# Optimization experiments

Measured on AMD Instinct MI355X. Metric: run time of the kernel, lower is better.

The kernel has to match this reference:

```python
import jax, jax.numpy as jnp
from jax import lax
import numpy as np

NBITS = 3  # PartialSumLSQ bit width


def binarize(x):
    # straight-through sign (Binarize in BNN code modifies .data -> identity STE)
    return x + lax.stop_gradient(jnp.sign(x) - x)


def lsq(y, alpha):
    # LSQ quantizer for partial sums: q = round(clamp(y/a, Qn, Qp)) * a, STE round,
    # gradient-scaled step size (forward value unaffected by g).
    Qn, Qp = -(2 ** (NBITS - 1)), 2 ** (NBITS - 1) - 1
    g = 1.0 / np.sqrt(y.size * Qp)
    a = alpha * g + lax.stop_gradient(alpha - alpha * g)
    yc = jnp.clip(y / a, Qn, Qp)
    yq = yc + lax.stop_gradient(jnp.round(yc) - yc)
    return yq * a


def split_slices(xp, cgroups):
    # xp: [B, 128*cgroups, H+2, W+2]; reproduces split_tensor_128/256/512 ordering:
    # channel group outermost, then col offset j, then row offset i.
    H, W = xp.shape[2] - 2, xp.shape[3] - 2
    sl = [xp[:, g * 128:(g + 1) * 128, i:i + H, j:j + W]
          for g in range(cgroups) for j in range(3) for i in range(3)]
    return jnp.stack(sl)  # [S, B, 128, H, W]


def psum_stage(x, w, b, alpha, cgroups):
    # emulated 3x3 binary conv: pad, split into S shifted 128-ch slices, per-slice
    # binarized 1x1 conv + bias, LSQ-quantize each partial sum, accumulate.
    xp = jnp.pad(binarize(x), ((0, 0), (0, 0), (1, 1), (1, 1)))
    xs = split_slices(xp, cgroups)                      # [S,B,128,H,W]
    y = jnp.einsum('sbchw,soc->sbohw', xs, binarize(w)) + b[:, None, :, None, None]
    return jax.vmap(lsq)(y, alpha).sum(0)               # [B,Cout,H,W]


def maxpool2(x):
    return lax.reduce_window(x, -jnp.inf, lax.max, (1, 1, 2, 2), (1, 1, 2, 2), 'VALID')


def bn(x, g, b):
    # eval-mode BatchNorm with running_mean=0, running_var=1 -> affine
    s = (1, -1) + (1,) * (x.ndim - 2)
    return x * g.reshape(s) + b.reshape(s)


def htanh(x):
    return jnp.clip(x, -1.0, 1.0)


def _forward(x, conv1_w, conv1_b, s2_w, s2_b, s2_a, s3_w, s3_b, s3_a,
             s4_w, s4_b, s4_a, s5_w, s5_b, s5_a, s6_w, s6_b, s6_a,
             bn1_g, bn1_b, bn2_g, bn2_b, bn3_g, bn3_b, bn4_g, bn4_b,
             bn5_g, bn5_b, bn6_g, bn6_b, fc1_w, fc1_b, fc2_w, fc2_b,
             fc3_w, fc3_b, fbn1_g, fbn1_b, fbn2_g, fbn2_b, fbn3_g, fbn3_b):
    # conv1: 3->128 3x3 pad1; input has 3 channels -> not binarized, weight binarized
    h = lax.conv_general_dilated(x, binarize(conv1_w), (1, 1), ((1, 1), (1, 1)),
                                 dimension_numbers=('NCHW', 'OIHW', 'NCHW'))
    h = h + conv1_b[None, :, None, None]
    h = htanh(bn(h, bn1_g, bn1_b))
    h = psum_stage(h, s2_w, s2_b, s2_a, 1)   # 128->128, 9 slices, 32x32
    h = maxpool2(h)                          # 16x16
    h = htanh(bn(h, bn2_g, bn2_b))
    h = psum_stage(h, s3_w, s3_b, s3_a, 1)   # 128->256, 9 slices
    h = htanh(bn(h, bn3_g, bn3_b))
    h = psum_stage(h, s4_w, s4_b, s4_a, 2)   # 256->256, 18 slices
    h = maxpool2(h)                          # 8x8
    h = htanh(bn(h, bn4_g, bn4_b))
    h = psum_stage(h, s5_w, s5_b, s5_a, 2)   # 256->512, 18 slices
    h = htanh(bn(h, bn5_g, bn5_b))
    h = psum_stage(h, s6_w, s6_b, s6_a, 4)   # 512->512, 36 slices
    h = maxpool2(h)                          # 4x4
    h = htanh(bn(h, bn6_g, bn6_b))
    # binarized classifier: 512*4*4 -> 1024 -> 1024 -> num_classes
    f = binarize(h.reshape(h.shape[0], -1))
    f = f @ binarize(fc1_w).T + fc1_b
    f = htanh(f * fbn1_g + fbn1_b)
    f = binarize(f) @ binarize(fc2_w).T + fc2_b
    f = htanh(f * fbn2_g + fbn2_b)
    f = binarize(f) @ binarize(fc3_w).T + fc3_b
    return f * fbn3_g + fbn3_b


def setup_inputs() -> dict:
    key = jax.random.key(0)
    ks = iter(jax.random.split(key, 80))
    def rn(shape, scale=1.0):
        return jax.random.normal(next(ks), shape, jnp.float32) * scale
    d = {}
    d['x'] = rn((64, 3, 32, 32))
    d['conv1_w'] = rn((128, 3, 3, 3), 0.1)
    d['conv1_b'] = rn((128,), 0.01)
    stages = {'s2': (9, 128), 's3': (9, 256), 's4': (18, 256),
              's5': (18, 512), 's6': (36, 512)}
    for name, (S, co) in stages.items():
        d[name + '_w'] = rn((S, co, 128), 0.1)
        d[name + '_b'] = rn((S, co), 0.01)
        d[name + '_a'] = jax.random.uniform(next(ks), (S,), jnp.float32, 0.05, 0.15)
    for i, c in zip(range(1, 7), [128, 128, 256, 256, 512, 512]):
        d[f'bn{i}_g'] = jnp.ones((c,), jnp.float32) + rn((c,), 0.01)
        d[f'bn{i}_b'] = rn((c,), 0.01)
    d['fc1_w'] = rn((1024, 512 * 16), 0.02); d['fc1_b'] = rn((1024,), 0.01)
    d['fc2_w'] = rn((1024, 1024), 0.02);     d['fc2_b'] = rn((1024,), 0.01)
    d['fc3_w'] = rn((10, 1024), 0.02);       d['fc3_b'] = rn((10,), 0.01)
    for i, c in zip(range(1, 4), [1024, 1024, 10]):
        d[f'fbn{i}_g'] = jnp.ones((c,), jnp.float32) + rn((c,), 0.01)
        d[f'fbn{i}_b'] = rn((c,), 0.01)
    return d


def reference(x, conv1_w, conv1_b, s2_w, s2_b, s2_a, s3_w, s3_b, s3_a,
              s4_w, s4_b, s4_a, s5_w, s5_b, s5_a, s6_w, s6_b, s6_a,
              bn1_g, bn1_b, bn2_g, bn2_b, bn3_g, bn3_b, bn4_g, bn4_b,
              bn5_g, bn5_b, bn6_g, bn6_b, fc1_w, fc1_b, fc2_w, fc2_b,
              fc3_w, fc3_b, fbn1_g, fbn1_b, fbn2_g, fbn2_b, fbn3_g, fbn3_b):
    return _forward(x, conv1_w, conv1_b, s2_w, s2_b, s2_a, s3_w, s3_b, s3_a,
                    s4_w, s4_b, s4_a, s5_w, s5_b, s5_a, s6_w, s6_b, s6_a,
                    bn1_g, bn1_b, bn2_g, bn2_b, bn3_g, bn3_b, bn4_g, bn4_b,
                    bn5_g, bn5_b, bn6_g, bn6_b, fc1_w, fc1_b, fc2_w, fc2_b,
                    fc3_w, fc3_b, fbn1_g, fbn1_b, fbn2_g, fbn2_b, fbn3_g, fbn3_b)
```

## Files before the change

### kernel.cpp

```cpp
#include <hip/hip_runtime.h>
#include <hip/hip_bf16.h>

typedef unsigned long long u64;

struct PackArgs {
    const float* w[7];
    u64* out[7];
    int cnt[7];
    int wpr[7];
    int nseg;
    int total;
};

__global__ void k_packall(PackArgs A) {
    int idx = blockIdx.x * blockDim.x + threadIdx.x;
    if (idx >= A.total) return;
    int seg = 0, base = 0, pre = 0;
    for (int t = 0; t < 7; ++t) {
        if (t < A.nseg) {
            if (idx >= pre) { seg = t; base = pre; }
            pre += A.cnt[t];
        }
    }
    int li = idx - base;
    int wpr = A.wpr[seg];
    int row = li / wpr, wi = li % wpr;
    const float* p = A.w[seg] + (size_t)row * wpr * 64 + (size_t)wi * 64;
    u64 m = 0;
    for (int j = 0; j < 64; ++j)
        if (p[j] > 0.f) m |= (1ull << j);
    A.out[seg][li] = m;
}

__global__ void k_packw_fc1(const float* __restrict__ w, u64* __restrict__ out) {
    int idx = blockIdx.x * blockDim.x + threadIdx.x;
    if (idx >= 1024 * 128) return;
    int row = idx >> 7, wd = idx & 127;
    int g = wd >> 5, h = (wd >> 3) & 3, x = (wd >> 1) & 3, k = wd & 1;
    const float* p = w + (size_t)row * 8192;
    u64 m = 0;
    for (int j = 0; j < 64; ++j) {
        int c = g * 128 + k * 64 + j;
        int f = c * 16 + h * 4 + x;
        if (p[f] > 0.f) m |= (1ull << j);
    }
    out[idx] = m;
}

struct LutArgs {
    const float* alpha[5];
    const float* bias[5];
    int off[5];
    int Cout[5];
    double ysize[5];
    int total;
};

__global__ void k_lutall(LutArgs A, double* __restrict__ lut) {
    int idx = blockIdx.x * blockDim.x + threadIdx.x;
    if (idx >= A.total) return;
    int seg = 0;
    for (int t = 1; t < 5; ++t) if (idx >= A.off[t]) seg = t;
    int li = idx - A.off[seg];
    int s = li / A.Cout[seg];
    double gq = 1.0 / sqrt(A.ysize[seg] * 3.0);
    double al = (double)A.alpha[seg][s];
    double tg = al * gq;
    double a  = tg + (al - tg);
    double b  = (double)A.bias[seg][li];
    double q0 = rint(fmin(fmax((0.0 + b) / a, -4.0), 3.0));
    double qp = rint(fmin(fmax((2.0 + b) / a, -4.0), 3.0));
    double qn = rint(fmin(fmax((-2.0 + b) / a, -4.0), 3.0));
    lut[(size_t)idx * 4 + 0] = qn * a;
    lut[(size_t)idx * 4 + 1] = q0 * a;
    lut[(size_t)idx * 4 + 2] = qp * a;
    lut[(size_t)idx * 4 + 3] = (qp == 3.0 && qn == -4.0) ? 0.0 : 1.0;
}

__global__ __launch_bounds__(128)
void k_conv1(const float* __restrict__ x, const float* __restrict__ w,
             const float* __restrict__ cb, const float* __restrict__ g1,
             const float* __restrict__ b1, u64* __restrict__ apack) {
    __shared__ double xs[3][3][34];
    int h = blockIdx.x & 31;
    int b = blockIdx.x >> 5;
    int tid = threadIdx.x;
    for (int idx = tid; idx < 306; idx += 128) {
        int dyy = idx / 102;
        int rem = idx - dyy * 102;
        int ci = rem / 34;
        int col = rem - ci * 34;
        int y = h + dyy - 1, xx = col - 1;
        double v = 0.0;
        if ((unsigned)y < 32u && (unsigned)xx < 32u)
            v = (double)x[((b * 3 + ci) * 32 + y) * 32 + xx];
        xs[dyy][ci][col] = v;
    }
    __syncthreads();
    int o = tid;
    double sg[3][3][3];
#pragma unroll
    for (int ci = 0; ci < 3; ++ci)
#pragma unroll
    for (int ky = 0; ky < 3; ++ky)
#pragma unroll
    for (int kx = 0; kx < 3; ++kx) {
        float wv = w[o * 27 + (ci * 3 + ky) * 3 + kx];
        sg[kx][ci][ky] = wv > 0.f ? 1.0 : (wv < 0.f ? -1.0 : 0.0);
    }
    double cbv = (double)cb[o], g1v = (double)g1[o], b1v = (double)b1[o];
    double A0 = 0.0, A1 = 0.0, A2 = 0.0;
    for (int pc = 0; pc < 34; ++pc) {
        double v[3][3];
#pragma unroll
        for (int ky = 0; ky < 3; ++ky)
#pragma unroll
        for (int ci = 0; ci < 3; ++ci)
            v[ky][ci] = xs[ky][ci][pc];
        A2 = 0.0;
#pragma unroll
        for (int ci = 0; ci < 3; ++ci)
#pragma unroll
        for (int ky = 0; ky < 3; ++ky) {
            A0 += v[ky][ci] * sg[2][ci][ky];
            A1 += v[ky][ci] * sg[1][ci][ky];
            A2 += v[ky][ci] * sg[0][ci][ky];
        }
        if (pc >= 2) {
            int wc = pc - 2;
            double t = (A0 + cbv) * g1v + b1v;
            u64 m = __ballot(t > 0.0);
            if ((tid & 63) == 0)
                apack[((size_t)(b * 1024 + h * 32 + wc)) * 2 + (tid >> 6)] = m;
        }
        A0 = A1; A1 = A2;
    }
}

template <int POOL, int G, int H, int W, int Cout, int OCHUNK, int NC>
__global__ __launch_bounds__(POOL * OCHUNK)
void k_stage(const u64* __restrict__ apack, const u64* __restrict__ wpack,
             const double* __restrict__ lut,
             const float* __restrict__ gam, const float* __restrict__ bet,
             u64* __restrict__ opack) {
    constexpr int CW = W / NC;
    constexpr int Ho = H / POOL, Wo = W / POOL;
    constexpr int NOC = Cout / OCHUNK;
    int bi = blockIdx.x;
    int oc = bi % NOC; bi /= NOC;
    int ch = bi % NC;  bi /= NC;
    int ph = bi % Ho;
    int b  = bi / Ho;
    int tid = threadIdx.x;
    int dy = tid / OCHUNK;
    int ol = tid - dy * OCHUNK;
    int o  = oc * OCHUNK + ol;
    int c0 = ch * CW;
    int y0 = ph * POOL + dy;

    double acc[CW];
#pragma unroll
    for (int c = 0; c < CW; ++c) acc[c] = 0.0;

    for (int g = 0; g < G; ++g) {
        const u64* gbase = apack + (size_t)(b * G + g) * H * W * 2;
#pragma unroll
        for (int j = 0; j < 3; ++j) {
#pragma unroll
            for (int i = 0; i < 3; ++i) {
                const int s = g * 9 + j * 3 + i;
                const size_t so = (size_t)s * Cout + o;
                const double* Lp = lut + so * 4;
                double cn = Lp[0], cz = Lp[1], cp = Lp[2];
                int y = y0 + i - 1;
                if ((unsigned)y >= (unsigned)H) {
#pragma unroll
                    for (int c = 0; c < CW; ++c) acc[c] += cz;
                    continue;
                }
                const u64* wp2 = wpack + so * 2;
                u64 w0 = wp2[0], w1 = wp2[1];
                const bool cutlo = (c0 == 0) && (j == 0);
                const bool cuthi = (c0 + CW == W) && (j == 2);
                if (cutlo) acc[0] += cz;
                if (cuthi) acc[CW - 1] += cz;
                const u64* p = gbase + ((size_t)y * W + (c0 + j - 1)) * 2;
#pragma unroll
                for (int c = 0; c < CW; ++c) {
                    if ((c > 0 || !cutlo) && (c < CW - 1 || !cuthi)) {
                        u64 a0 = p[2 * c], a1 = p[2 * c + 1];
                        int d = __popcll(a0 ^ w0) + __popcll(a1 ^ w1);
                        double v = (d < 64) ? cp : ((d > 64) ? cn : cz);
                        acc[c] += v;
                    }
                }
            }
        }
    }

    double gv = (double)gam[o], bv = (double)bet[o];
    if constexpr (POOL == 1) {
#pragma unroll
        for (int c = 0; c < CW; ++c) {
            double t = acc[c] * gv + bv;
            u64 bm = __ballot(t > 0.0);
            if ((tid & 63) == 0) {
                int pw = c0 + c;
                opack[(((size_t)(b * (Cout >> 7) + (o >> 7)) * Ho + ph) * Wo + pw) * 2
                      + ((o >> 6) & 1)] = bm;
            }
        }
    } else {
        __shared__ double pl[POOL][OCHUNK][CW / 2 + 1];
#pragma unroll
        for (int c2 = 0; c2 < CW / 2; ++c2)
            pl[dy][ol][c2] = fmax(acc[2 * c2], acc[2 * c2 + 1]);
        __syncthreads();
        if (dy == 0) {
#pragma unroll
            for (int c2 = 0; c2 < CW / 2; ++c2) {
                double m = fmax(pl[0][ol][c2], pl[1][ol][c2]);
                double t = m * gv + bv;
                u64 bm = __ballot(t > 0.0);
                if ((tid & 63) == 0) {
                    int pw = c0 / 2 + c2;
                    opack[(((size_t)(b * (Cout >> 7) + (o >> 7)) * Ho + ph) * Wo + pw) * 2
                          + ((o >> 6) & 1)] = bm;
                }
            }
        }
    }
}

__global__ void k_fc_pack(const u64* __restrict__ apack, const u64* __restrict__ wpack,
                          const float* __restrict__ bias, const float* __restrict__ gam,
                          const float* __restrict__ bet, u64* __restrict__ opack,
                          int nw, int Rwords) {
    int wg = blockIdx.x % Rwords;
    int b = blockIdx.x / Rwords;
    int r = wg * 64 + threadIdx.x;
    const u64* a = apack + (size_t)b * nw;
    const u64* wp = wpack + (size_t)r * nw;
    int d = 0;
    for (int i = 0; i < nw; ++i) d += __popcll(a[i] ^ wp[i]);
    double isum = (double)(nw * 64 - 2 * d);
    double t = (isum + (double)bias[r]) * (double)gam[r] + (double)bet[r];
    u64 m = __ballot(t > 0.0);
    if (threadIdx.x == 0) opack[(size_t)b * Rwords + wg] = m;
}

__global__ void k_fc3(const u64* __restrict__ apack, const u64* __restrict__ wpack,
                      const float* __restrict__ bias, const float* __restrict__ gam,
                      const float* __restrict__ bet, float* __restrict__ out) {
    int idx = blockIdx.x * blockDim.x + threadIdx.x;
    if (idx >= 640) return;
    int b = idx / 10, r = idx % 10;
    const u64* a = apack + (size_t)b * 16;
    const u64* wp = wpack + (size_t)r * 16;
    int d = 0;
    for (int i = 0; i < 16; ++i) d += __popcll(a[i] ^ wp[i]);
    double isum = (double)(1024 - 2 * d);
    out[idx] = (float)((isum + (double)bias[r]) * (double)gam[r] + (double)bet[r]);
}


extern "C" void kernel_launch(void* const* d_in, const int* in_sizes, int n_in,
                              void* d_out, int out_size, void* d_ws, size_t ws_size,
                              hipStream_t stream) {
    const float* x       = (const float*)d_in[0];
    const float* conv1_w = (const float*)d_in[1];
    const float* conv1_b = (const float*)d_in[2];
    const float* s_w[5]  = {(const float*)d_in[3], (const float*)d_in[6], (const float*)d_in[9],
                            (const float*)d_in[12], (const float*)d_in[15]};
    const float* s_b[5]  = {(const float*)d_in[4], (const float*)d_in[7], (const float*)d_in[10],
                            (const float*)d_in[13], (const float*)d_in[16]};
    const float* s_a[5]  = {(const float*)d_in[5], (const float*)d_in[8], (const float*)d_in[11],
                            (const float*)d_in[14], (const float*)d_in[17]};
    const float* bn_g[6], *bn_b[6];
    for (int i = 0; i < 6; ++i) { bn_g[i] = (const float*)d_in[18 + 2 * i]; bn_b[i] = (const float*)d_in[19 + 2 * i]; }
    const float* fc1_w = (const float*)d_in[30]; const float* fc1_b = (const float*)d_in[31];
    const float* fc2_w = (const float*)d_in[32]; const float* fc2_b = (const float*)d_in[33];
    const float* fc3_w = (const float*)d_in[34]; const float* fc3_b = (const float*)d_in[35];
    const float* fbn_g[3], *fbn_b[3];
    for (int i = 0; i < 3; ++i) { fbn_g[i] = (const float*)d_in[36 + 2 * i]; fbn_b[i] = (const float*)d_in[37 + 2 * i]; }

    size_t off = 0;
    auto alloc = [&](size_t bytes) { off = (off + 255) & ~(size_t)255; size_t o = off; off += bytes; return o; };
    char* ws = (char*)d_ws;
    size_t o_apA = alloc(1048576);
    size_t o_apB = alloc(1048576);
    size_t o_wp  = alloc((size_t)71424 * 8);
    size_t o_lut = alloc((size_t)35712 * 4 * 8);
    size_t o_wf1 = alloc((size_t)1024 * 128 * 8);
    size_t o_wf2 = alloc((size_t)1024 * 16 * 8);
    size_t o_wf3 = alloc((size_t)10 * 16 * 8);
    size_t o_fp1 = alloc((size_t)64 * 16 * 8);
    size_t o_fp2 = alloc((size_t)64 * 16 * 8);
    if (off > ws_size) return;

    u64* apA = (u64*)(ws + o_apA);
    u64* apB = (u64*)(ws + o_apB);
    u64* wpbuf = (u64*)(ws + o_wp);
    double* lutbuf = (double*)(ws + o_lut);
    u64* wf1 = (u64*)(ws + o_wf1);
    u64* wf2 = (u64*)(ws + o_wf2);
    u64* wf3 = (u64*)(ws + o_wf3);
    u64* fp1 = (u64*)(ws + o_fp1);
    u64* fp2 = (u64*)(ws + o_fp2);

    const int rowoff[5] = {0, 1152, 3456, 8064, 17280};
    u64* wp[5];  double* lut[5];
    for (int i = 0; i < 5; ++i) {
        wp[i]  = wpbuf + (size_t)rowoff[i] * 2;
        lut[i] = lutbuf + (size_t)rowoff[i] * 4;
    }

    PackArgs PA;
    const int scnt[5] = {2304, 4608, 9216, 18432, 36864};
    int tot = 0;
    for (int i = 0; i < 5; ++i) { PA.w[i] = s_w[i]; PA.out[i] = wp[i]; PA.cnt[i] = scnt[i]; PA.wpr[i] = 2; tot += scnt[i]; }
    PA.w[5] = fc2_w; PA.out[5] = wf2; PA.cnt[5] = 1024 * 16; PA.wpr[5] = 16; tot += 1024 * 16;
    PA.w[6] = fc3_w; PA.out[6] = wf3; PA.cnt[6] = 10 * 16;   PA.wpr[6] = 16; tot += 10 * 16;
    PA.nseg = 7; PA.total = tot;
    k_packall<<<(tot + 255) / 256, 256, 0, stream>>>(PA);
    k_packw_fc1<<<(1024 * 128 + 255) / 256, 256, 0, stream>>>(fc1_w, wf1);

    LutArgs LA;
    const int sCout[5] = {128, 256, 256, 512, 512};
    const double sYsz[5] = {8388608.0, 4194304.0, 4194304.0, 2097152.0, 2097152.0};
    for (int i = 0; i < 5; ++i) {
        LA.alpha[i] = s_a[i]; LA.bias[i] = s_b[i];
        LA.off[i] = rowoff[i]; LA.Cout[i] = sCout[i]; LA.ysize[i] = sYsz[i];
    }
    LA.total = 35712;
    k_lutall<<<(35712 + 255) / 256, 256, 0, stream>>>(LA, lutbuf);

    k_conv1<<<64 * 32, 128, 0, stream>>>(x, conv1_w, conv1_b, bn_g[0], bn_b[0], apA);

    k_stage<2, 1, 32, 32, 128, 128, 2><<<64 * 16 * 2, 256, 0, stream>>>(
        apA, wp[0], lut[0], bn_g[1], bn_b[1], apB);
    k_stage<1, 1, 16, 16, 256, 256, 1><<<64 * 16, 256, 0, stream>>>(
        apB, wp[1], lut[1], bn_g[2], bn_b[2], apA);
    k_stage<2, 2, 16, 16, 256, 256, 2><<<64 * 8 * 2, 512, 0, stream>>>(
        apA, wp[2], lut[2], bn_g[3], bn_b[3], apB);
    k_stage<1, 2, 8, 8, 512, 512, 1><<<64 * 8, 512, 0, stream>>>(
        apB, wp[3], lut[3], bn_g[4], bn_b[4], apA);
    k_stage<2, 4, 8, 8, 512, 256, 1><<<64 * 4 * 2, 512, 0, stream>>>(
        apA, wp[4], lut[4], bn_g[5], bn_b[5], apB);

    k_fc_pack<<<64 * 16, 64, 0, stream>>>(apB, wf1, fc1_b, fbn_g[0], fbn_b[0], fp1, 128, 16);
    k_fc_pack<<<64 * 16, 64, 0, stream>>>(fp1, wf2, fc2_b, fbn_g[1], fbn_b[1], fp2, 16, 16);
    k_fc3<<<10, 64, 0, stream>>>(fp2, wf3, fc3_b, fbn_g[2], fbn_b[2], (float*)d_out);
}
```

Before: 264.2 us.

## Stage activations in LDS, fold zero-case LUT into bias, wave-ballot weight packing

Each stage kernel now copies its activation tile, halo included, into shared memory once per block, and the popcount loop reads from there instead of global memory. The LUT is cut to two deltas relative to the zero case, and the summed zero-case constant goes into a per-channel init from a new k_cz kernel, so padding slices no longer need explicit adds. Weight packing uses wave ballots with coalesced loads, and fc1 weights are packed transposed so the FC reads are coalesced. Several stages also switch to NC=2 column splits for more blocks. The risks are extra LDS pressure, the added kernel launch, and the changed FP summation order of the zero-case constants.

```diff
diff --git a/kernel.cpp b/kernel.cpp
--- a/kernel.cpp
+++ b/kernel.cpp
@@ -7,44 +7,52 @@
     const float* w[7];
     u64* out[7];
     int cnt[7];
-    int wpr[7];
-    int nseg;
     int total;
 };
 
 __global__ void k_packall(PackArgs A) {
-    int idx = blockIdx.x * blockDim.x + threadIdx.x;
-    if (idx >= A.total) return;
+    int gid = blockIdx.x * blockDim.x + threadIdx.x;
+    int wid = gid >> 6;
+    int lane = threadIdx.x & 63;
+    if (wid >= A.total) return;
     int seg = 0, base = 0, pre = 0;
+#pragma unroll
     for (int t = 0; t < 7; ++t) {
-        if (t < A.nseg) {
-            if (idx >= pre) { seg = t; base = pre; }
-            pre += A.cnt[t];
-        }
-    }
-    int li = idx - base;
-    int wpr = A.wpr[seg];
-    int row = li / wpr, wi = li % wpr;
-    const float* p = A.w[seg] + (size_t)row * wpr * 64 + (size_t)wi * 64;
-    u64 m = 0;
-    for (int j = 0; j < 64; ++j)
-        if (p[j] > 0.f) m |= (1ull << j);
-    A.out[seg][li] = m;
-}
-
-__global__ void k_packw_fc1(const float* __restrict__ w, u64* __restrict__ out) {
-    int idx = blockIdx.x * blockDim.x + threadIdx.x;
-    if (idx >= 1024 * 128) return;
-    int row = idx >> 7, wd = idx & 127;
-    int g = wd >> 5, h = (wd >> 3) & 3, x = (wd >> 1) & 3, k = wd & 1;
-    const float* p = w + (size_t)row * 8192;
-    u64 m = 0;
-    for (int j = 0; j < 64; ++j) {
-        int c = g * 128 + k * 64 + j;
-        int f = c * 16 + h * 4 + x;
-        if (p[f] > 0.f) m |= (1ull << j);
-    }
-    out[idx] = m;
+        if (wid >= pre) { seg = t; base = pre; }
+        pre += A.cnt[t];
+    }
+    int li = wid - base;
+    const float* p = A.w[seg] + ((size_t)li << 6);
+    u64 m = __ballot(p[lane] > 0.f);
+    if (lane == 0) A.out[seg][li] = m;
+}
+
+__global__ void k_packw_fc1(const float* __restrict__ w, u64* __restrict__ outT) {
+    int gid = blockIdx.x * blockDim.x + threadIdx.x;
+    int wid = gid >> 6;
+    int lane = threadIdx.x & 63;
+    if (wid >= 1024 * 8) return;
+    int row = wid >> 3, gk = wid & 7;
+    int g = gk >> 1, k = gk & 1;
+    int c = g * 128 + k * 64 + lane;
+    const float* p = w + (size_t)row * 8192 + (size_t)c * 16;
+    float arr[16];
+#pragma unroll
+    for (int q = 0; q < 4; ++q) {
+        float4 f = ((const float4*)p)[q];
+        arr[4 * q + 0] = f.x; arr[4 * q + 1] = f.y;
+        arr[4 * q + 2] = f.z; arr[4 * q + 3] = f.w;
+    }
+#pragma unroll
+    for (int h = 0; h < 4; ++h)
+#pragma unroll
+    for (int xq = 0; xq < 4; ++xq) {
+        u64 m = __ballot(arr[h * 4 + xq] > 0.f);
+        if (lane == 0) {
+            int wd = g * 32 + h * 8 + xq * 2 + k;
+            outT[(size_t)wd * 1024 + row] = m;
+        }
+    }
 }
 
 struct LutArgs {
@@ -56,10 +64,11 @@
     int total;
 };
 
-__global__ void k_lutall(LutArgs A, double* __restrict__ lut) {
+__global__ void k_lutall(LutArgs A, double* __restrict__ lut2) {
     int idx = blockIdx.x * blockDim.x + threadIdx.x;
     if (idx >= A.total) return;
     int seg = 0;
+#pragma unroll
     for (int t = 1; t < 5; ++t) if (idx >= A.off[t]) seg = t;
     int li = idx - A.off[seg];
     int s = li / A.Cout[seg];
@@ -68,13 +77,42 @@
     double tg = al * gq;
     double a  = tg + (al - tg);
     double b  = (double)A.bias[seg][li];
-    double q0 = rint(fmin(fmax((0.0 + b) / a, -4.0), 3.0));
+    double q0 = rint(fmin(fmax(b / a, -4.0), 3.0));
     double qp = rint(fmin(fmax((2.0 + b) / a, -4.0), 3.0));
     double qn = rint(fmin(fmax((-2.0 + b) / a, -4.0), 3.0));
-    lut[(size_t)idx * 4 + 0] = qn * a;
-    lut[(size_t)idx * 4 + 1] = q0 * a;
-    lut[(size_t)idx * 4 + 2] = qp * a;
-    lut[(size_t)idx * 4 + 3] = (qp == 3.0 && qn == -4.0) ? 0.0 : 1.0;
+    double cz = q0 * a;
+    lut2[(size_t)idx * 2 + 0] = qp * a - cz;
+    lut2[(size_t)idx * 2 + 1] = qn * a - cz;
+}
+
+struct CzArgs {
+    const float* alpha[5];
+    const float* bias[5];
+    int off[5];
+    int S[5];
+    int Cout[5];
+    double ysize[5];
+    int total;
+};
+
+__global__ void k_cz(CzArgs A, double* __restrict__ czv) {
+    int idx = blockIdx.x * blockDim.x + threadIdx.x;
+    if (idx >= A.total) return;
+    int seg = 0;
+#pragma unroll
+    for (int t = 1; t < 5; ++t) if (idx >= A.off[t]) seg = t;
+    int o = idx - A.off[seg];
+    double gq = 1.0 / sqrt(A.ysize[seg] * 3.0);
+    double CZ = 0.0;
+    for (int s = 0; s < A.S[seg]; ++s) {
+        double al = (double)A.alpha[seg][s];
+        double tg = al * gq;
+        double a  = tg + (al - tg);
+        double b  = (double)A.bias[seg][s * A.Cout[seg] + o];
+        double q0 = rint(fmin(fmax(b / a, -4.0), 3.0));
+        CZ += q0 * a;
+    }
+    czv[idx] = CZ;
 }
 
 __global__ __launch_bounds__(128)
@@ -140,12 +178,21 @@
 template <int POOL, int G, int H, int W, int Cout, int OCHUNK, int NC>
 __global__ __launch_bounds__(POOL * OCHUNK)
 void k_stage(const u64* __restrict__ apack, const u64* __restrict__ wpack,
-             const double* __restrict__ lut,
+             const double* __restrict__ lut2, const double* __restrict__ czv,
              const float* __restrict__ gam, const float* __restrict__ bet,
              u64* __restrict__ opack) {
     constexpr int CW = W / NC;
     constexpr int Ho = H / POOL, Wo = W / POOL;
     constexpr int NOC = Cout / OCHUNK;
+    constexpr int NROW = POOL + 2;
+    constexpr int NCOL = CW + 2;
+    constexpr int NT = POOL * OCHUNK;
+    __shared__ alignas(16) u64 sact[G][NROW][NCOL][2];
+    constexpr int PLP = (POOL == 2) ? 2 : 1;
+    constexpr int PLO = (POOL == 2) ? OCHUNK : 1;
+    constexpr int PLC = (POOL == 2) ? (CW / 2) : 1;
+    __shared__ double pl[PLP][PLO][PLC];
+
     int bi = blockIdx.x;
     int oc = bi % NOC; bi /= NOC;
     int ch = bi % NC;  bi /= NC;
@@ -156,43 +203,54 @@
     int ol = tid - dy * OCHUNK;
     int o  = oc * OCHUNK + ol;
     int c0 = ch * CW;
-    int y0 = ph * POOL + dy;
-
+    int ybase = ph * POOL - 1;
+
+    constexpr int NWD = G * NROW * NCOL;
+    for (int t = tid; t < NWD; t += NT) {
+        int g = t / (NROW * NCOL);
+        int rr = t - g * (NROW * NCOL);
+        int yy = rr / NCOL;
+        int xx = rr - yy * NCOL;
+        int y = ybase + yy, x = c0 - 1 + xx;
+        u64 v0 = 0, v1 = 0;
+        if ((unsigned)y < (unsigned)H && (unsigned)x < (unsigned)W) {
+            const u64* p = apack + (((size_t)((b * G + g) * H + y)) * W + x) * 2;
+            v0 = p[0]; v1 = p[1];
+        }
+        sact[g][yy][xx][0] = v0;
+        sact[g][yy][xx][1] = v1;
+    }
+    __syncthreads();
+
+    double CZ = czv[o];
     double acc[CW];
 #pragma unroll
-    for (int c = 0; c < CW; ++c) acc[c] = 0.0;
-
+    for (int c = 0; c < CW; ++c) acc[c] = CZ;
+
+#pragma unroll
     for (int g = 0; g < G; ++g) {
-        const u64* gbase = apack + (size_t)(b * G + g) * H * W * 2;
 #pragma unroll
         for (int j = 0; j < 3; ++j) {
 #pragma unroll
             for (int i = 0; i < 3; ++i) {
-                const int s = g * 9 + j * 3 + i;
-                const size_t so = (size_t)s * Cout + o;
-                const double* Lp = lut + so * 4;
-                double cn = Lp[0], cz = Lp[1], cp = Lp[2];
-                int y = y0 + i - 1;
-                if ((unsigned)y >= (unsigned)H) {
-#pragma unroll
-                    for (int c = 0; c < CW; ++c) acc[c] += cz;
-                    continue;
-                }
-                const u64* wp2 = wpack + so * 2;
-                u64 w0 = wp2[0], w1 = wp2[1];
-                const bool cutlo = (c0 == 0) && (j == 0);
-                const bool cuthi = (c0 + CW == W) && (j == 2);
-                if (cutlo) acc[0] += cz;
-                if (cuthi) acc[CW - 1] += cz;
-                const u64* p = gbase + ((size_t)y * W + (c0 + j - 1)) * 2;
+                int s = g * 9 + j * 3 + i;
+                int y = ph * POOL + dy + i - 1;
+                if ((unsigned)y >= (unsigned)H) continue;
+                size_t so = (size_t)s * Cout + o;
+                u64 w0 = wpack[so * 2], w1 = wpack[so * 2 + 1];
+                double dp = lut2[so * 2], dn = lut2[so * 2 + 1];
+                bool cutlo = (ch == 0) && (j == 0);
+                bool cuthi = (ch == NC - 1) && (j == 2);
+                int yy = dy + i;
 #pragma unroll
                 for (int c = 0; c < CW; ++c) {
-                    if ((c > 0 || !cutlo) && (c < CW - 1 || !cuthi)) {
-                        u64 a0 = p[2 * c], a1 = p[2 * c + 1];
-                        int d = __popcll(a0 ^ w0) + __popcll(a1 ^ w1);
-                        double v = (d < 64) ? cp : ((d > 64) ? cn : cz);
-                        acc[c] += v;
-                    }
+                    if ((c == 0 && cutlo) || (c == CW - 1 && cuthi)) continue;
+                    u64 a0 = sact[g][yy][c + j][0];
+                    u64 a1 = sact[g][yy][c + j][1];
+                    int d = __popcll(a0 ^ w0) + __popcll(a1 ^ w1);
+                    double val = (d < 64) ? dp : dn;
+                    val = (d == 64) ? 0.0 : val;
+                    acc[c] += val;
                 }
             }
         }
@@ -211,7 +269,6 @@
             }
         }
     } else {
-        __shared__ double pl[POOL][OCHUNK][CW / 2 + 1];
 #pragma unroll
         for (int c2 = 0; c2 < CW / 2; ++c2)
             pl[dy][ol][c2] = fmax(acc[2 * c2], acc[2 * c2 + 1]);
@@ -233,6 +290,7 @@
 }
 
 __global__ void k_fc_pack(const u64* __restrict__ apack, const u64* __restrict__ wpack,
+                          int rstride, int wstride,
                           const float* __restrict__ bias, const float* __restrict__ gam,
                           const float* __restrict__ bet, u64* __restrict__ opack,
                           int nw, int Rwords) {
@@ -240,9 +298,9 @@
     int b = blockIdx.x / Rwords;
     int r = wg * 64 + threadIdx.x;
     const u64* a = apack + (size_t)b * nw;
-    const u64* wp = wpack + (size_t)r * nw;
+    const u64* wp = wpack + (size_t)r * rstride;
     int d = 0;
-    for (int i = 0; i < nw; ++i) d += __popcll(a[i] ^ wp[i]);
+    for (int i = 0; i < nw; ++i) d += __popcll(a[i] ^ wp[(size_t)i * wstride]);
     double isum = (double)(nw * 64 - 2 * d);
     double t = (isum + (double)bias[r]) * (double)gam[r] + (double)bet[r];
     u64 m = __ballot(t > 0.0);
@@ -290,10 +348,11 @@
     size_t o_apA = alloc(1048576);
     size_t o_apB = alloc(1048576);
     size_t o_wp  = alloc((size_t)71424 * 8);
-    size_t o_lut = alloc((size_t)35712 * 4 * 8);
+    size_t o_lut = alloc((size_t)35712 * 2 * 8);
+    size_t o_cz  = alloc((size_t)1664 * 8);
     size_t o_wf1 = alloc((size_t)1024 * 128 * 8);
     size_t o_wf2 = alloc((size_t)1024 * 16 * 8);
-    size_t o_wf3 = alloc((size_t)10 * 16 * 8);
+    size_t o_wf3 = alloc((size_t)10 * 16 * 8 + 256);
     size_t o_fp1 = alloc((size_t)64 * 16 * 8);
     size_t o_fp2 = alloc((size_t)64 * 16 * 8);
     if (off > ws_size) return;
@@ -301,31 +360,38 @@
     u64* apA = (u64*)(ws + o_apA);
     u64* apB = (u64*)(ws + o_apB);
     u64* wpbuf = (u64*)(ws + o_wp);
-    double* lutbuf = (double*)(ws + o_lut);
-    u64* wf1 = (u64*)(ws + o_wf1);
+    double* lut2 = (double*)(ws + o_lut);
+    double* czbuf = (double*)(ws + o_cz);
+    u64* wf1T = (u64*)(ws + o_wf1);
     u64* wf2 = (u64*)(ws + o_wf2);
     u64* wf3 = (u64*)(ws + o_wf3);
     u64* fp1 = (u64*)(ws + o_fp1);
     u64* fp2 = (u64*)(ws + o_fp2);
 
     const int rowoff[5] = {0, 1152, 3456, 8064, 17280};
-    u64* wp[5];  double* lut[5];
+    const int czoff[5]  = {0, 128, 384, 640, 1152};
+    u64* wp[5];  double* lt[5];  double* cz[5];
     for (int i = 0; i < 5; ++i) {
-        wp[i]  = wpbuf + (size_t)rowoff[i] * 2;
-        lut[i] = lutbuf + (size_t)rowoff[i] * 4;
+        wp[i] = wpbuf + (size_t)rowoff[i] * 2;
+        lt[i] = lut2 + (size_t)rowoff[i] * 2;
+        cz[i] = czbuf + czoff[i];
     }
 
     PackArgs PA;
     const int scnt[5] = {2304, 4608, 9216, 18432, 36864};
     int tot = 0;
-    for (int i = 0; i < 5; ++i) { PA.w[i] = s_w[i]; PA.out[i] = wp[i]; PA.cnt[i] = scnt[i]; PA.wpr[i] = 2; tot += scnt[i]; }
-    PA.w[5] = fc2_w; PA.out[5] = wf2; PA.cnt[5] = 1024 * 16; PA.wpr[5] = 16; tot += 1024 * 16;
-    PA.w[6] = fc3_w; PA.out[6] = wf3; PA.cnt[6] = 10 * 16;   PA.wpr[6] = 16; tot += 10 * 16;
-    PA.nseg = 7; PA.total = tot;
-    k_packall<<<(tot + 255) / 256, 256, 0, stream>>>(PA);
-    k_packw_fc1<<<(1024 * 128 + 255) / 256, 256, 0, stream>>>(fc1_w, wf1);
+    for (int i = 0; i < 5; ++i) { PA.w[i] = s_w[i]; PA.out[i] = wp[i]; PA.cnt[i] = scnt[i]; tot += scnt[i]; }
+    PA.w[5] = fc2_w; PA.out[5] = wf2; PA.cnt[5] = 1024 * 16; tot += 1024 * 16;
+    PA.w[6] = fc3_w; PA.out[6] = wf3; PA.cnt[6] = 160;       tot += 160;
+    PA.total = tot;
+    {
+        long long thr = (long long)tot * 64;
+        k_packall<<<(int)((thr + 255) / 256), 256, 0, stream>>>(PA);
+    }
+    k_packw_fc1<<<(1024 * 8 * 64) / 256, 256, 0, stream>>>(fc1_w, wf1T);
 
     LutArgs LA;
+    const int sS[5]    = {9, 9, 18, 18, 36};
     const int sCout[5] = {128, 256, 256, 512, 512};
     const double sYsz[5] = {8388608.0, 4194304.0, 4194304.0, 2097152.0, 2097152.0};
     for (int i = 0; i < 5; ++i) {
@@ -333,22 +399,30 @@
         LA.off[i] = rowoff[i]; LA.Cout[i] = sCout[i]; LA.ysize[i] = sYsz[i];
     }
     LA.total = 35712;
-    k_lutall<<<(35712 + 255) / 256, 256, 0, stream>>>(LA, lutbuf);
+    k_lutall<<<(35712 + 255) / 256, 256, 0, stream>>>(LA, lut2);
+
+    CzArgs CA;
+    for (int i = 0; i < 5; ++i) {
+        CA.alpha[i] = s_a[i]; CA.bias[i] = s_b[i];
+        CA.off[i] = czoff[i]; CA.S[i] = sS[i]; CA.Cout[i] = sCout[i]; CA.ysize[i] = sYsz[i];
+    }
+    CA.total = 1664;
+    k_cz<<<(1664 + 255) / 256, 256, 0, stream>>>(CA, czbuf);
 
     k_conv1<<<64 * 32, 128, 0, stream>>>(x, conv1_w, conv1_b, bn_g[0], bn_b[0], apA);
 
     k_stage<2, 1, 32, 32, 128, 128, 2><<<64 * 16 * 2, 256, 0, stream>>>(
-        apA, wp[0], lut[0], bn_g[1], bn_b[1], apB);
-    k_stage<1, 1, 16, 16, 256, 256, 1><<<64 * 16, 256, 0, stream>>>(
-        apB, wp[1], lut[1], bn_g[2], bn_b[2], apA);
+        apA, wp[0], lt[0], cz[0], bn_g[1], bn_b[1], apB);
+    k_stage<1, 1, 16, 16, 256, 256, 2><<<64 * 16 * 2, 256, 0, stream>>>(
+        apB, wp[1], lt[1], cz[1], bn_g[2], bn_b[2], apA);
     k_stage<2, 2, 16, 16, 256, 256, 2><<<64 * 8 * 2, 512, 0, stream>>>(
-        apA, wp[2], lut[2], bn_g[3], bn_b[3], apB);
-    k_stage<1, 2, 8, 8, 512, 512, 1><<<64 * 8, 512, 0, stream>>>(
-        apB, wp[3], lut[3], bn_g[4], bn_b[4], apA);
-    k_stage<2, 4, 8, 8, 512, 256, 1><<<64 * 4 * 2, 512, 0, stream>>>(
-        apA, wp[4], lut[4], bn_g[5], bn_b[5], apB);
-
-    k_fc_pack<<<64 * 16, 64, 0, stream>>>(apB, wf1, fc1_b, fbn_g[0], fbn_b[0], fp1, 128, 16);
-    k_fc_pack<<<64 * 16, 64, 0, stream>>>(fp1, wf2, fc2_b, fbn_g[1], fbn_b[1], fp2, 16, 16);
+        apA, wp[2], lt[2], cz[2], bn_g[3], bn_b[3], apB);
+    k_stage<1, 2, 8, 8, 512, 512, 2><<<64 * 8 * 2, 512, 0, stream>>>(
+        apB, wp[3], lt[3], cz[3], bn_g[4], bn_b[4], apA);
+    k_stage<2, 4, 8, 8, 512, 256, 2><<<64 * 4 * 2 * 2, 512, 0, stream>>>(
+        apA, wp[4], lt[4], cz[4], bn_g[5], bn_b[5], apB);
+
+    k_fc_pack<<<64 * 16, 64, 0, stream>>>(apB, wf1T, 1, 1024, fc1_b, fbn_g[0], fbn_b[0], fp1, 128, 16);
+    k_fc_pack<<<64 * 16, 64, 0, stream>>>(fp1, wf2, 16, 1, fc2_b, fbn_g[1], fbn_b[1], fp2, 16, 16);
     k_fc3<<<10, 64, 0, stream>>>(fp2, wf3, fc3_b, fbn_g[2], fbn_b[2], (float*)d_out);
 }
```

Result: faster. 237.3 us (-10.2%).
